# Kernel optimization log

Hardware: AMD Instinct MI355X
Metric: run time of the kernel (lower is better)

The kernel has to match this reference:

```python
import jax, jax.numpy as jnp
import numpy as np
from jax import lax

R = 8  # REGION_NUM_

def _avgpool3(x):
    # AvgPool2d(kernel=H-2*(H//3), stride=H//3) -> exactly 3x3 spatial output
    H = x.shape[2]
    s = H // 3
    k = H - 2 * s
    y = lax.reduce_window(x, 0.0, lax.add, (1, 1, k, k), (1, 1, s, s), 'VALID')
    return y / float(k * k)

def _hist_drconv(x, hist, wa, ba, wb, bb, out_ch):
    # x: [B,Cin,H,W], hist: [B,R,H,W]
    B, Cin, H, W = x.shape
    p = _avgpool3(x)                                                     # [B,Cin,3,3]
    h = jax.nn.sigmoid(jnp.einsum('bchw,oc->bohw', p, wa) + ba[None, :, None, None])  # [B,R*R,3,3]
    hg = h.reshape(B, R, R, 3, 3)
    wbg = wb.reshape(R, Cin * out_ch, R)                                 # grouped 1x1 conv, groups=R
    kern = jnp.einsum('brchw,roc->brohw', hg, wbg) + bb.reshape(1, R, Cin * out_ch, 1, 1)
    ki = kern.reshape(B, R * out_ch, Cin, 3, 3)                          # per-sample dynamic kernels
    def per_sample(xi, kb):
        # xi: [Cin,H,W], kb: [R*out,Cin,3,3] -> [R*out,H,W]
        return lax.conv_general_dilated(xi[None], kb, (1, 1), [(1, 1), (1, 1)])[0]
    y = jax.vmap(per_sample)(x, ki)                                      # [B,R*out,H,W]
    y = y.reshape(B, R, out_ch, H, W)
    # asign_index: one-hot of argmax over regions, select-sum
    mask = jax.nn.one_hot(jnp.argmax(hist, axis=1), R, axis=1, dtype=y.dtype)  # [B,R,H,W]
    return (y * mask[:, :, None]).sum(axis=1)                            # [B,out,H,W]

def _bn_relu(y, g, b, m, v):
    scale = (g / jnp.sqrt(v + 1e-5))[None, :, None, None]
    return jax.nn.relu((y - m[None, :, None, None]) * scale + b[None, :, None, None])

def setup_inputs() -> dict:
    key = jax.random.key(0)
    ks = jax.random.split(key, 20)
    B, Cin, Cmid, Cout, H = 8, 8, 8, 8, 256
    f32 = jnp.float32
    d = {}
    d['x'] = jax.random.normal(ks[0], (B, Cin, H, H), f32)
    d['histmap'] = jax.random.uniform(ks[1], (B, R, H, H), dtype=f32)
    d['w1a'] = jax.random.normal(ks[2], (R * R, Cin), f32) * 0.1
    d['b1a'] = jax.random.normal(ks[3], (R * R,), f32) * 0.1
    d['w1b'] = jax.random.normal(ks[4], (R * Cin * Cmid, R), f32) * 0.1
    d['b1b'] = jax.random.normal(ks[5], (R * Cin * Cmid,), f32) * 0.1
    d['g1'] = jax.random.uniform(ks[6], (Cmid,), dtype=f32) + 0.5
    d['be1'] = jax.random.normal(ks[7], (Cmid,), f32) * 0.1
    d['m1'] = jax.random.normal(ks[8], (Cmid,), f32) * 0.1
    d['v1'] = jax.random.uniform(ks[9], (Cmid,), dtype=f32) + 0.5
    d['w2a'] = jax.random.normal(ks[10], (R * R, Cmid), f32) * 0.1
    d['b2a'] = jax.random.normal(ks[11], (R * R,), f32) * 0.1
    d['w2b'] = jax.random.normal(ks[12], (R * Cmid * Cout, R), f32) * 0.1
    d['b2b'] = jax.random.normal(ks[13], (R * Cmid * Cout,), f32) * 0.1
    d['g2'] = jax.random.uniform(ks[14], (Cout,), dtype=f32) + 0.5
    d['be2'] = jax.random.normal(ks[15], (Cout,), f32) * 0.1
    d['m2'] = jax.random.normal(ks[16], (Cout,), f32) * 0.1
    d['v2'] = jax.random.uniform(ks[17], (Cout,), dtype=f32) + 0.5
    return d

def reference(x, histmap, w1a, b1a, w1b, b1b, g1, be1, m1, v1,
              w2a, b2a, w2b, b2b, g2, be2, m2, v2):
    y = _hist_drconv(x, histmap, w1a, b1a, w1b, b1b, 8)
    y = _bn_relu(y, g1, be1, m1, v1)
    y = _hist_drconv(y, histmap, w2a, b2a, w2b, b2b, 8)
    return _bn_relu(y, g2, be2, m2, v2)
```

## Files before the change

kernel.cpp:

```cpp
#include <hip/hip_runtime.h>
#include <math.h>


#define HWPX 65536
#define HDIM 256

typedef __fp16 h2v __attribute__((ext_vector_type(2)));
typedef __fp16 v8h __attribute__((ext_vector_type(8)));
typedef float v4f __attribute__((ext_vector_type(4)));

union UH { uint u; h2v h; };
union U4V8 { uint4 u4; v8h h8; };

__global__ __launch_bounds__(256) void prep_kernel(const float* __restrict__ x,
                                                   const float* __restrict__ hist,
                                                   float* __restrict__ rs1,
                                                   uint4* __restrict__ xh4,
                                                   unsigned char* __restrict__ regmap) {
  int u = blockIdx.x, t = threadIdx.x, w = t >> 6, l = t & 63;
  if (u < 512) {
    int b = u & 7, rg = u >> 3;
    int row = rg * 4 + w;
    const float* base = x + (size_t)b * 8 * HWPX + row * HDIM + l * 4;
    float4 ch[8];
#pragma unroll
    for (int c = 0; c < 8; c++) ch[c] = *(const float4*)(base + (size_t)c * HWPX);
    uint4* dst = xh4 + ((size_t)b * 256 + row) * 256 + l * 4;
#pragma unroll
    for (int p = 0; p < 4; p++) {
      UH h0, h1, h2, h3;
      h0.h = __builtin_amdgcn_cvt_pkrtz((&ch[0].x)[p], (&ch[1].x)[p]);
      h1.h = __builtin_amdgcn_cvt_pkrtz((&ch[2].x)[p], (&ch[3].x)[p]);
      h2.h = __builtin_amdgcn_cvt_pkrtz((&ch[4].x)[p], (&ch[5].x)[p]);
      h3.h = __builtin_amdgcn_cvt_pkrtz((&ch[6].x)[p], (&ch[7].x)[p]);
      dst[p] = make_uint4(h0.u, h1.u, h2.u, h3.u);
    }
#pragma unroll
    for (int c = 0; c < 8; c++) {
      float s0 = 0.f, s1 = 0.f, s2 = 0.f;
#pragma unroll
      for (int p = 0; p < 4; p++) {
        int px = l * 4 + p;
        float val = (&ch[c].x)[p];
        if (px <= 85) s0 += val;
        if (px >= 85 && px <= 170) s1 += val;
        if (px >= 170) s2 += val;
      }
#pragma unroll
      for (int off = 32; off >= 1; off >>= 1) {
        s0 += __shfl_xor(s0, off);
        s1 += __shfl_xor(s1, off);
        s2 += __shfl_xor(s2, off);
      }
      if (l == 0) {
        float* q = rs1 + ((size_t)(b * 8 + c) * 256 + row) * 3;
        q[0] = s0; q[1] = s1; q[2] = s2;
      }
    }
  } else {
    int u2 = u - 512;
    int b = u2 & 7, rg = u2 >> 3;
    int row = rg * 4 + w;
    int x0 = l * 4;
    const float* hp = hist + (size_t)b * 8 * HWPX + row * HDIM + x0;
    float4 hv[8];
#pragma unroll
    for (int r = 0; r < 8; r++) hv[r] = *(const float4*)(hp + (size_t)r * HWPX);
    uchar4 rg4;
#pragma unroll
    for (int p = 0; p < 4; p++) {
      float best = (&hv[0].x)[p];
      int reg = 0;
#pragma unroll
      for (int r = 1; r < 8; r++) {
        float q = (&hv[r].x)[p];
        if (q > best) { best = q; reg = r; }
      }
      (&rg4.x)[p] = (unsigned char)reg;
    }
    *(uchar4*)(regmap + (size_t)b * HWPX + row * HDIM + x0) = rg4;
  }
}

template <int LAYER>
__global__ __launch_bounds__(256, 2) void conv_kernel(
    const uint4* __restrict__ in4, const unsigned char* __restrict__ regmap,
    const float* __restrict__ rs,
    const float* __restrict__ wa, const float* __restrict__ ba,
    const float* __restrict__ wb, const float* __restrict__ bb,
    const float* __restrict__ g, const float* __restrict__ be,
    const float* __restrict__ m, const float* __restrict__ v,
    uint* __restrict__ outh, float* __restrict__ outf,
    float* __restrict__ rs2out) {
  __shared__ uint4 xs[6][260];
  __shared__ __align__(16) float Dbuf[4][64][20];
  __shared__ uint4 Bf[4][3][64];
  __shared__ float pp[72][3];
  __shared__ float pP[8][9];
  __shared__ float hh[576];
  __shared__ float bns[8], bnsh[8];
  __shared__ unsigned char rm[4][256];

  int bid = blockIdx.x;
  int b = bid & 7, rg = bid >> 3, r0 = rg * 4;
  int t = threadIdx.x, w = t >> 6, l = t & 63;

  for (int i = t; i < 6 * 256; i += 256) {
    int dy = i >> 8, px = i & 255;
    int yy = r0 - 1 + dy;
    uint4 val = make_uint4(0, 0, 0, 0);
    if ((unsigned)yy < 256u) val = in4[((size_t)b * 256 + yy) * 256 + px];
    xs[dy][px + 1] = val;
  }
  if (t < 12) {
    int rr = t % 6, cc = (t < 6) ? 0 : 257;
    xs[rr][cc] = make_uint4(0, 0, 0, 0);
  }
  ((uint*)rm)[t] = *(const uint*)(regmap + (size_t)b * HWPX + (r0 + (t >> 6)) * HDIM + (t & 63) * 4);

  if (t < 216) {
    int u = t / 3, part = t - 3 * (t / 3);
    int c = u / 9, ij = u % 9, i = ij / 3, j = ij % 3;
    int rr0 = 85 * i + part * 29;
    int cnt = (part == 2) ? 28 : 29;
    const float* q = rs + ((size_t)(b * 8 + c) * 256 + rr0) * 3 + j;
    float s = 0.f;
    for (int k = 0; k < cnt; k++) s += q[k * 3];
    pp[u][part] = s;
  }
  if (t >= 248) {
    int oc = t - 248;
    float s = g[oc] * rsqrtf(v[oc] + 1e-5f);
    bns[oc] = s;
    bnsh[oc] = be[oc] - m[oc] * s;
  }
  __syncthreads();
  if (t < 72) pP[t / 9][t % 9] = (pp[t][0] + pp[t][1] + pp[t][2]) * (1.f / 7396.f);
  __syncthreads();
  for (int u = t; u < 576; u += 256) {
    int o = u / 9, ij = u - o * 9;
    float z = ba[o];
#pragma unroll
    for (int c = 0; c < 8; c++) z += pP[c][ij] * wa[o * 8 + c];
    hh[u] = 1.f / (1.f + expf(-z));
  }
  __syncthreads();
  {
    int nt = t >> 6, l2 = t & 63;
    int n = nt * 16 + (l2 & 15);
    int reg = n >> 3, oc = n & 7;
#pragma unroll
    for (int ks = 0; ks < 3; ks++) {
      int tap = ks * 4 + (l2 >> 4);
      uint4 rec = make_uint4(0, 0, 0, 0);
      if (tap < 9) {
        float hv[8];
#pragma unroll
        for (int cc = 0; cc < 8; cc++) hv[cc] = hh[(reg * 8 + cc) * 9 + tap];
        float vj[8];
#pragma unroll
        for (int j = 0; j < 8; j++) {
          int rowk = reg * 64 + oc * 8 + j;
          float val = bb[rowk];
#pragma unroll
          for (int cc = 0; cc < 8; cc++) val += hv[cc] * wb[rowk * 8 + cc];
          vj[j] = val;
        }
        UH p0, p1, p2, p3;
        p0.h = __builtin_amdgcn_cvt_pkrtz(vj[0], vj[1]);
        p1.h = __builtin_amdgcn_cvt_pkrtz(vj[2], vj[3]);
        p2.h = __builtin_amdgcn_cvt_pkrtz(vj[4], vj[5]);
        p3.h = __builtin_amdgcn_cvt_pkrtz(vj[6], vj[7]);
        rec = make_uint4(p0.u, p1.u, p2.u, p3.u);
      }
      Bf[nt][ks][l2] = rec;
    }
  }
  __syncthreads();

  U4V8 Bfr[4][3];
#pragma unroll
  for (int nt = 0; nt < 4; nt++)
#pragma unroll
    for (int ks = 0; ks < 3; ks++)
      Bfr[nt][ks].u4 = Bf[nt][ks][l];

  int row = r0 + w;
  int ocp = l >> 4;
  float bn_s0 = bns[2 * ocp], bn_h0 = bnsh[2 * ocp];
  float bn_s1 = bns[2 * ocp + 1], bn_h1 = bnsh[2 * ocp + 1];
  float rsm[2][3] = {{0.f, 0.f, 0.f}, {0.f, 0.f, 0.f}};

  for (int mt = 0; mt < 16; mt++) {
    U4V8 A[3];
#pragma unroll
    for (int ks = 0; ks < 3; ks++) {
      int tap = ks * 4 + (l >> 4);
      if (tap > 8) tap = 8;
      int dy = tap / 3, dx = tap - dy * 3;
      A[ks].u4 = xs[w + dy][mt * 16 + (l & 15) + dx];
    }
    v4f acc[4];
#pragma unroll
    for (int nt = 0; nt < 4; nt++) {
      v4f z = {0.f, 0.f, 0.f, 0.f};
      z = __builtin_amdgcn_mfma_f32_16x16x32_f16(A[0].h8, Bfr[nt][0].h8, z, 0, 0, 0);
      z = __builtin_amdgcn_mfma_f32_16x16x32_f16(A[1].h8, Bfr[nt][1].h8, z, 0, 0, 0);
      z = __builtin_amdgcn_mfma_f32_16x16x32_f16(A[2].h8, Bfr[nt][2].h8, z, 0, 0, 0);
      acc[nt] = z;
    }
#pragma unroll
    for (int nt = 0; nt < 4; nt++) {
      int col = nt * 16 + (l & 15);
      int px0 = (l >> 4) * 4;
      *(v4f*)&Dbuf[w][col][px0] = acc[nt];
    }
    int gx = l & 15;
    int px = mt * 16 + gx;
    int reg = rm[w][px];
    int c0 = reg * 8 + ocp * 2;
    float o0 = Dbuf[w][c0][gx];
    float o1 = Dbuf[w][c0 + 1][gx];
    o0 = fmaxf(o0 * bn_s0 + bn_h0, 0.f);
    o1 = fmaxf(o1 * bn_s1 + bn_h1, 0.f);
    if (LAYER == 1) {
      UH pk;
      pk.h = __builtin_amdgcn_cvt_pkrtz(o0, o1);
      outh[(((size_t)b * 256 + row) * 256 + px) * 4 + ocp] = pk.u;
      if (px <= 85)               { rsm[0][0] += o0; rsm[1][0] += o1; }
      if (px >= 85 && px <= 170)  { rsm[0][1] += o0; rsm[1][1] += o1; }
      if (px >= 170)              { rsm[0][2] += o0; rsm[1][2] += o1; }
    } else {
      outf[((size_t)(b * 8 + 2 * ocp)) * HWPX + row * HDIM + px] = o0;
      outf[((size_t)(b * 8 + 2 * ocp + 1)) * HWPX + row * HDIM + px] = o1;
    }
  }

  if (LAYER == 1) {
#pragma unroll
    for (int i = 0; i < 2; i++)
#pragma unroll
      for (int j = 0; j < 3; j++) {
#pragma unroll
        for (int off = 1; off <= 8; off <<= 1)
          rsm[i][j] += __shfl_xor(rsm[i][j], off);
      }
    if ((l & 15) == 0) {
#pragma unroll
      for (int i = 0; i < 2; i++) {
        float* q = rs2out + ((size_t)(b * 8 + 2 * ocp + i) * 256 + row) * 3;
        q[0] = rsm[i][0]; q[1] = rsm[i][1]; q[2] = rsm[i][2];
      }
    }
  }
}

extern "C" void kernel_launch(void* const* d_in, const int* in_sizes, int n_in,
                              void* d_out, int out_size, void* d_ws, size_t ws_size,
                              hipStream_t stream) {
  const float* x    = (const float*)d_in[0];
  const float* hist = (const float*)d_in[1];
  const float* w1a  = (const float*)d_in[2];
  const float* b1a  = (const float*)d_in[3];
  const float* w1b  = (const float*)d_in[4];
  const float* b1b  = (const float*)d_in[5];
  const float* g1   = (const float*)d_in[6];
  const float* be1  = (const float*)d_in[7];
  const float* m1   = (const float*)d_in[8];
  const float* v1   = (const float*)d_in[9];
  const float* w2a  = (const float*)d_in[10];
  const float* b2a  = (const float*)d_in[11];
  const float* w2b  = (const float*)d_in[12];
  const float* b2b  = (const float*)d_in[13];
  const float* g2   = (const float*)d_in[14];
  const float* be2  = (const float*)d_in[15];
  const float* m2   = (const float*)d_in[16];
  const float* v2   = (const float*)d_in[17];
  float* outp = (float*)d_out;

  char* ws = (char*)d_ws;
  unsigned char* regmap = (unsigned char*)ws;
  uint4* xh4  = (uint4*)(ws + 524288);
  uint4* y1h4 = (uint4*)(ws + 8912896);
  float* rs1 = (float*)(ws + 17301504);
  float* rs2 = (float*)(ws + 17399808);

  prep_kernel<<<1024, 256, 0, stream>>>(x, hist, rs1, xh4, regmap);
  conv_kernel<1><<<512, 256, 0, stream>>>(xh4, regmap, rs1, w1a, b1a, w1b, b1b,
                                          g1, be1, m1, v1, (uint*)y1h4, nullptr, rs2);
  conv_kernel<2><<<512, 256, 0, stream>>>(y1h4, regmap, rs2, w2a, b2a, w2b, b2b,
                                          g2, be2, m2, v2, nullptr, outp, nullptr);
}
```

Baseline: 65.27 us.

## Double-buffer MFMA result staging with swizzled LDS and union-shared scratch

The per-tile LDS staging buffer is now double-buffered, so the gather, BN and store for tile mt-1 run after the MFMAs for tile mt are issued, removing the same-iteration write-then-read dependency. The staging layout uses an XOR swizzle on the column index to spread LDS bank accesses, and the setup scratch arrays share storage with the larger Dbuf through a union, with an added barrier before reuse. The mt loop is fully unrolled. This raises register and code size, and the rs2 workspace offset moves, which risks occupancy and correctness if the layout assumptions are wrong.

```diff
diff --git a/kernel.cpp b/kernel.cpp
--- a/kernel.cpp
+++ b/kernel.cpp
@@ -92,12 +92,16 @@
     const float* __restrict__ m, const float* __restrict__ v,
     uint* __restrict__ outh, float* __restrict__ outf,
     float* __restrict__ rs2out) {
-  __shared__ uint4 xs[6][260];
-  __shared__ __align__(16) float Dbuf[4][64][20];
-  __shared__ uint4 Bf[4][3][64];
-  __shared__ float pp[72][3];
-  __shared__ float pP[8][9];
-  __shared__ float hh[576];
+  __shared__ uint4 xs[6][258];
+  __shared__ union {
+    struct {
+      float pp[72][3];
+      float pP[8][9];
+      float hh[576];
+      uint4 Bf[4][3][64];
+    } a;
+    float Dbuf[8192];
+  } su;
   __shared__ float bns[8], bnsh[8];
   __shared__ unsigned char rm[4][256];
 
@@ -126,7 +130,7 @@
     const float* q = rs + ((size_t)(b * 8 + c) * 256 + rr0) * 3 + j;
     float s = 0.f;
     for (int k = 0; k < cnt; k++) s += q[k * 3];
-    pp[u][part] = s;
+    su.a.pp[u][part] = s;
   }
   if (t >= 248) {
     int oc = t - 248;
@@ -135,14 +139,14 @@
     bnsh[oc] = be[oc] - m[oc] * s;
   }
   __syncthreads();
-  if (t < 72) pP[t / 9][t % 9] = (pp[t][0] + pp[t][1] + pp[t][2]) * (1.f / 7396.f);
+  if (t < 72) su.a.pP[t / 9][t % 9] = (su.a.pp[t][0] + su.a.pp[t][1] + su.a.pp[t][2]) * (1.f / 7396.f);
   __syncthreads();
   for (int u = t; u < 576; u += 256) {
     int o = u / 9, ij = u - o * 9;
     float z = ba[o];
 #pragma unroll
-    for (int c = 0; c < 8; c++) z += pP[c][ij] * wa[o * 8 + c];
-    hh[u] = 1.f / (1.f + expf(-z));
+    for (int c = 0; c < 8; c++) z += su.a.pP[c][ij] * wa[o * 8 + c];
+    su.a.hh[u] = 1.f / (1.f + expf(-z));
   }
   __syncthreads();
   {
@@ -156,7 +160,7 @@
       if (tap < 9) {
         float hv[8];
 #pragma unroll
-        for (int cc = 0; cc < 8; cc++) hv[cc] = hh[(reg * 8 + cc) * 9 + tap];
+        for (int cc = 0; cc < 8; cc++) hv[cc] = su.a.hh[(reg * 8 + cc) * 9 + tap];
         float vj[8];
 #pragma unroll
         for (int j = 0; j < 8; j++) {
@@ -173,7 +177,7 @@
         p3.h = __builtin_amdgcn_cvt_pkrtz(vj[6], vj[7]);
         rec = make_uint4(p0.u, p1.u, p2.u, p3.u);
       }
-      Bf[nt][ks][l2] = rec;
+      su.a.Bf[nt][ks][l2] = rec;
     }
   }
   __syncthreads();
@@ -183,14 +187,45 @@
   for (int nt = 0; nt < 4; nt++)
 #pragma unroll
     for (int ks = 0; ks < 3; ks++)
-      Bfr[nt][ks].u4 = Bf[nt][ks][l];
+      Bfr[nt][ks].u4 = su.a.Bf[nt][ks][l];
+  __syncthreads();
 
   int row = r0 + w;
   int ocp = l >> 4;
+  int gx = l & 15;
   float bn_s0 = bns[2 * ocp], bn_h0 = bnsh[2 * ocp];
   float bn_s1 = bns[2 * ocp + 1], bn_h1 = bnsh[2 * ocp + 1];
   float rsm[2][3] = {{0.f, 0.f, 0.f}, {0.f, 0.f, 0.f}};
 
+  int dbbase = w * 64 * 16;
+
+#define DSLOT(s) (su.Dbuf + (s) * 4 * 64 * 16 + dbbase)
+
+#define GATHER(j)                                                              \
+  {                                                                            \
+    int px = (j) * 16 + gx;                                                    \
+    int reg = rm[w][px];                                                       \
+    int c0 = reg * 8 + ocp * 2;                                                \
+    float* D = DSLOT((j) & 1);                                                 \
+    int blk0 = (gx & ~3) ^ (((c0 >> 1) & 3) << 2);                             \
+    float o0 = D[c0 * 16 + blk0 + (gx & 3)];                                   \
+    float o1 = D[(c0 + 1) * 16 + blk0 + (gx & 3)];                             \
+    o0 = fmaxf(o0 * bn_s0 + bn_h0, 0.f);                                       \
+    o1 = fmaxf(o1 * bn_s1 + bn_h1, 0.f);                                       \
+    if (LAYER == 1) {                                                          \
+      UH pk;                                                                   \
+      pk.h = __builtin_amdgcn_cvt_pkrtz(o0, o1);                               \
+      outh[(((size_t)b * 256 + row) * 256 + px) * 4 + ocp] = pk.u;             \
+      if (px <= 85)              { rsm[0][0] += o0; rsm[1][0] += o1; }         \
+      if (px >= 85 && px <= 170) { rsm[0][1] += o0; rsm[1][1] += o1; }         \
+      if (px >= 170)             { rsm[0][2] += o0; rsm[1][2] += o1; }         \
+    } else {                                                                   \
+      outf[((size_t)(b * 8 + 2 * ocp)) * HWPX + row * HDIM + px] = o0;         \
+      outf[((size_t)(b * 8 + 2 * ocp + 1)) * HWPX + row * HDIM + px] = o1;     \
+    }                                                                          \
+  }
+
+#pragma unroll
   for (int mt = 0; mt < 16; mt++) {
     U4V8 A[3];
 #pragma unroll
@@ -209,32 +244,21 @@
       z = __builtin_amdgcn_mfma_f32_16x16x32_f16(A[2].h8, Bfr[nt][2].h8, z, 0, 0, 0);
       acc[nt] = z;
     }
-#pragma unroll
-    for (int nt = 0; nt < 4; nt++) {
-      int col = nt * 16 + (l & 15);
+    {
+      float* D = DSLOT(mt & 1);
       int px0 = (l >> 4) * 4;
-      *(v4f*)&Dbuf[w][col][px0] = acc[nt];
-    }
-    int gx = l & 15;
-    int px = mt * 16 + gx;
-    int reg = rm[w][px];
-    int c0 = reg * 8 + ocp * 2;
-    float o0 = Dbuf[w][c0][gx];
-    float o1 = Dbuf[w][c0 + 1][gx];
-    o0 = fmaxf(o0 * bn_s0 + bn_h0, 0.f);
-    o1 = fmaxf(o1 * bn_s1 + bn_h1, 0.f);
-    if (LAYER == 1) {
-      UH pk;
-      pk.h = __builtin_amdgcn_cvt_pkrtz(o0, o1);
-      outh[(((size_t)b * 256 + row) * 256 + px) * 4 + ocp] = pk.u;
-      if (px <= 85)               { rsm[0][0] += o0; rsm[1][0] += o1; }
-      if (px >= 85 && px <= 170)  { rsm[0][1] += o0; rsm[1][1] += o1; }
-      if (px >= 170)              { rsm[0][2] += o0; rsm[1][2] += o1; }
-    } else {
-      outf[((size_t)(b * 8 + 2 * ocp)) * HWPX + row * HDIM + px] = o0;
-      outf[((size_t)(b * 8 + 2 * ocp + 1)) * HWPX + row * HDIM + px] = o1;
-    }
-  }
+#pragma unroll
+      for (int nt = 0; nt < 4; nt++) {
+        int col = nt * 16 + (l & 15);
+        int idx = col * 16 + (px0 ^ (((col >> 1) & 3) << 2));
+        *(v4f*)&D[idx] = acc[nt];
+      }
+    }
+    if (mt > 0) GATHER(mt - 1);
+  }
+  GATHER(15);
+#undef GATHER
+#undef DSLOT
 
   if (LAYER == 1) {
 #pragma unroll
@@ -283,7 +307,7 @@
   uint4* xh4  = (uint4*)(ws + 524288);
   uint4* y1h4 = (uint4*)(ws + 8912896);
   float* rs1 = (float*)(ws + 17301504);
-  float* rs2 = (float*)(ws + 17399808);
+  float* rs2 = (float*)(ws + 17498112);
 
   prep_kernel<<<1024, 256, 0, stream>>>(x, hist, rs1, xh4, regmap);
   conv_kernel<1><<<512, 256, 0, stream>>>(xh4, regmap, rs1, w1a, b1a, w1b, b1b,
```

Result: no change. 66.35 us (+1.7%).
